# Kernel optimization log

Hardware: AMD Instinct MI355X
Metric: run time of the kernel (lower is better)

The kernel has to match this reference:

```python
import jax, jax.numpy as jnp
import numpy as np

BS, C, H, W = 2, 256, 64, 64
CH = C // 8  # hidden channels = 32


def conv1(x, w, b):
    # 1x1 conv: w [out,in], b [out], x [b,in,H,W] -> [b,out,H,W]
    return jnp.einsum('oc,bchw->bohw', w, x) + b[None, :, None, None]


def setup_inputs() -> dict:
    key = jax.random.key(0)
    ks = jax.random.split(key, 32)
    d = {}
    d['x'] = jax.random.normal(ks[0], (BS, C, H, W), dtype=jnp.float32)
    d['y'] = jax.random.normal(ks[1], (BS, C, H, W), dtype=jnp.float32)
    i = 2
    def wproj(shape):
        nonlocal i
        w = jax.random.normal(ks[i], shape, dtype=jnp.float32) * 0.05
        i += 1
        return w
    for nm in ['f1', 'g1', 'h1', 'f2', 'g2', 'h2']:
        d['w' + nm] = wproj((CH, C))
        d['b' + nm] = jnp.zeros((CH,), dtype=jnp.float32)
    for nm in ['v11', 'v12', 'v21', 'v22']:
        d['w' + nm] = wproj((C, CH))
        d['b' + nm] = jnp.zeros((C,), dtype=jnp.float32)
    for nm in ['o1', 'o2']:
        d['w' + nm] = wproj((C, 2 * C))
        d['b' + nm] = jnp.zeros((C,), dtype=jnp.float32)
    return d


def reference(x, y, wf1, bf1, wg1, bg1, wh1, bh1, wf2, bf2, wg2, bg2, wh2, bh2,
              wv11, bv11, wv12, bv12, wv21, bv21, wv22, bv22, wo1, bo1, wo2, bo2):
    bs, c, h, w = x.shape
    n = h * w
    f1 = conv1(x, wf1, bf1).reshape(bs, -1, n)  # [b,ch,n]
    g1 = conv1(x, wg1, bg1).reshape(bs, -1, n)
    f2 = conv1(y, wf2, bf2).reshape(bs, -1, n)
    g2 = conv1(y, wg2, bg2).reshape(bs, -1, n)
    # attn = softmax(f^T g) over last dim, [b,n,n]
    attn11 = jax.nn.softmax(jnp.einsum('bcn,bcm->bnm', f1, g1), axis=-1)
    attn12 = jax.nn.softmax(jnp.einsum('bcn,bcm->bnm', f1, g2), axis=-1)
    attn21 = jax.nn.softmax(jnp.einsum('bcn,bcm->bnm', f2, g1), axis=-1)
    attn22 = jax.nn.softmax(jnp.einsum('bcn,bcm->bnm', f2, g2), axis=-1)
    h1 = conv1(x, wh1, bh1).reshape(bs, -1, n)  # note: both h from x, as in source
    h2 = conv1(x, wh2, bh2).reshape(bs, -1, n)
    # bmm(h, attn^T): out[c,m] = sum_n h[c,n] attn[m,n]
    v11 = conv1(jnp.einsum('bcn,bmn->bcm', h1, attn11).reshape(bs, -1, h, w), wv11, bv11)
    v12 = conv1(jnp.einsum('bcn,bmn->bcm', h2, attn12).reshape(bs, -1, h, w), wv12, bv12)
    v21 = conv1(jnp.einsum('bcn,bmn->bcm', h1, attn21).reshape(bs, -1, h, w), wv21, bv21)
    v22 = conv1(jnp.einsum('bcn,bmn->bcm', h2, attn22).reshape(bs, -1, h, w), wv22, bv22)
    x_out = x + conv1(jnp.concatenate([v11, v12], axis=1), wo1, bo1)
    y_out = y + conv1(jnp.concatenate([v21, v22], axis=1), wo2, bo2)
    return (x_out, y_out)
```

## Files before the change

### kernel.cpp

```cpp
#include <hip/hip_runtime.h>
#include <hip/hip_bf16.h>
#include <cstdint>

#define N 4096
#define CC 256
#define CH 32
#define L2E 1.4426950408889634f

typedef __attribute__((ext_vector_type(8)))  short short8;
typedef __attribute__((ext_vector_type(16))) float f32x16;
typedef __attribute__((ext_vector_type(4)))  uint32_t u32x4;

#define OFF_WFRAG 0
#define OFF_WEFF  311296
#define OFF_BEFF  344064
#define OFF_QF    344576
#define OFF_KF    606720
#define OFF_VF    868864

__device__ __forceinline__ uint32_t cvtpk_bf16(float lo, float hi) {
  uint32_t r;
  asm("v_cvt_pk_bf16_f32 %0, %1, %2" : "=v"(r) : "v"(lo), "v"(hi));
  return r;
}

__device__ __forceinline__ void rows_to_frags(const float* p, u32x4& lo, u32x4& hi) {
#pragma unroll
  for (int kh = 0; kh < 2; ++kh) {
    int base = kh * 8;
    uint32_t x0 = cvtpk_bf16(p[base + 0], p[base + 1]);
    uint32_t y0 = cvtpk_bf16(p[base + 4], p[base + 5]);
    asm volatile("v_permlane32_swap_b32 %0, %1" : "+v"(x0), "+v"(y0));
    uint32_t x1 = cvtpk_bf16(p[base + 2], p[base + 3]);
    uint32_t y1 = cvtpk_bf16(p[base + 6], p[base + 7]);
    asm volatile("v_permlane32_swap_b32 %0, %1" : "+v"(x1), "+v"(y1));
    u32x4 r; r[0] = x0; r[1] = x1; r[2] = y0; r[3] = y1;
    if (kh == 0) lo = r; else hi = r;
  }
}

__device__ __forceinline__ void attn_step(short8 ak0, short8 ak1, short8 bv0, short8 bv1,
                                          short8 bq0, short8 bq1,
                                          f32x16& ao, float& lacc, const f32x16& zero16) {
  f32x16 sa = __builtin_amdgcn_mfma_f32_32x32x16_bf16(ak0, bq0, zero16, 0, 0, 0);
  sa = __builtin_amdgcn_mfma_f32_32x32x16_bf16(ak1, bq1, sa, 0, 0, 0);
  float p[16];
#pragma unroll
  for (int r = 0; r < 16; ++r) p[r] = __builtin_amdgcn_exp2f(sa[r]);
  float t0 = 0.f, t1 = 0.f;
#pragma unroll
  for (int r = 0; r < 8; ++r) { t0 += p[2 * r]; t1 += p[2 * r + 1]; }
  lacc += t0 + t1;
  u32x4 lo, hi;
  rows_to_frags(p, lo, hi);
  ao = __builtin_amdgcn_mfma_f32_32x32x16_bf16(__builtin_bit_cast(short8, lo), bv0, ao, 0, 0, 0);
  ao = __builtin_amdgcn_mfma_f32_32x32x16_bf16(__builtin_bit_cast(short8, hi), bv1, ao, 0, 0, 0);
}

__global__ void k_prep2(const float* __restrict__ wf1, const float* __restrict__ wg1,
                        const float* __restrict__ wh1, const float* __restrict__ wf2,
                        const float* __restrict__ wg2, const float* __restrict__ wh2,
                        const float* __restrict__ wo1, const float* __restrict__ wo2,
                        const float* __restrict__ wv11, const float* __restrict__ wv12,
                        const float* __restrict__ wv21, const float* __restrict__ wv22,
                        const float* __restrict__ bv11, const float* __restrict__ bv12,
                        const float* __restrict__ bv21, const float* __restrict__ bv22,
                        const float* __restrict__ bo1, const float* __restrict__ bo2,
                        uint16_t* __restrict__ wfragb, float* __restrict__ weff,
                        float* __restrict__ beff) {
  int bid = blockIdx.x;
  if (bid < 192) {
    int idx = bid * 256 + threadIdx.x;
    int q = idx >> 13, kb = (idx >> 9) & 15, l = (idx >> 3) & 63, j = idx & 7;
    int ch = l & 31, c = kb * 16 + (l >> 5) * 8 + j;
    const float* w = q == 0 ? wf1 : q == 1 ? wg1 : q == 2 ? wh1
                   : q == 3 ? wf2 : q == 4 ? wg2 : wh2;
    wfragb[idx] = (uint16_t)cvtpk_bf16(w[ch * CC + c], 0.f);
  } else if (bid < 320) {
    int bid2 = bid - 192;
    int r = bid2 >> 6, ch = bid2 & 63, half = ch >> 5, chp = ch & 31;
    int o = threadIdx.x;
    const float* wv = (r == 0) ? (half ? wv12 : wv11) : (half ? wv22 : wv21);
    const float* wrow = (r == 0 ? wo1 : wo2) + (size_t)o * 512 + half * 256;
    float a[8];
#pragma unroll
    for (int u = 0; u < 8; ++u) a[u] = 0.f;
#pragma unroll 4
    for (int c = 0; c < 256; c += 8) {
#pragma unroll
      for (int u = 0; u < 8; ++u)
        a[u] = fmaf(wrow[c + u], wv[(c + u) * CH + chp], a[u]);
    }
    weff[((size_t)r * 64 + ch) * 256 + o] =
        ((a[0] + a[1]) + (a[2] + a[3])) + ((a[4] + a[5]) + (a[6] + a[7]));
  } else {
    int r = bid - 320;
    int o = threadIdx.x;
    const float* bo  = r == 0 ? bo1 : bo2;
    const float* bva = r == 0 ? bv11 : bv21;
    const float* bvb = r == 0 ? bv12 : bv22;
    const float* wrow = (r == 0 ? wo1 : wo2) + (size_t)o * 512;
    float a[4], b4[4];
#pragma unroll
    for (int u = 0; u < 4; ++u) { a[u] = 0.f; b4[u] = 0.f; }
#pragma unroll 8
    for (int c = 0; c < 256; c += 4) {
#pragma unroll
      for (int u = 0; u < 4; ++u) {
        a[u]  = fmaf(wrow[c + u],       bva[c + u], a[u]);
        b4[u] = fmaf(wrow[c + u + 256], bvb[c + u], b4[u]);
      }
    }
    beff[r * 256 + o] = bo[o] + ((a[0] + a[1]) + (a[2] + a[3]))
                              + ((b4[0] + b4[1]) + (b4[2] + b4[3]));
  }
}

__global__ __launch_bounds__(256) void k_proj(
    const float* __restrict__ x, const float* __restrict__ y,
    const uint16_t* __restrict__ wfragb,
    const float* __restrict__ bf1, const float* __restrict__ bg1, const float* __restrict__ bh1,
    const float* __restrict__ bf2, const float* __restrict__ bg2, const float* __restrict__ bh2,
    uint16_t* __restrict__ Qf, uint16_t* __restrict__ Kf, uint16_t* __restrict__ Vf) {
  int bid = blockIdx.x;
  int w = __builtin_amdgcn_readfirstlane(threadIdx.x >> 6);
  int l = threadIdx.x & 63, l31 = l & 31, l5 = l >> 5;

  int q, ql, b, nt, inst;
  const float* src;
  const float* bias;
  bool isf, isV;
  if (bid < 256) {
    ql = w; b = bid >> 7; nt = bid & 127;
    src = x; inst = 0;
    q = (ql == 3) ? 5 : ql;
    isf = (ql == 0); isV = (ql >= 2);
    bias = ql == 0 ? bf1 : ql == 1 ? bg1 : ql == 2 ? bh1 : bh2;
  } else {
    int u = (bid - 256) * 4 + w;
    int chunk = u >> 1; ql = u & 1;
    b = chunk >> 7; nt = chunk & 127;
    src = y; inst = 1;
    q = 3 + ql;
    isf = (ql == 0); isV = false;
    bias = ql == 0 ? bf2 : bg2;
  }

  const u32x4* wp = (const u32x4*)wfragb + (size_t)q * 16 * 64 + l;
  u32x4 wfr[16];
#pragma unroll
  for (int kb = 0; kb < 16; ++kb) wfr[kb] = wp[kb * 64];

  const float* sp = src + (size_t)b * CC * N + (size_t)(l5 * 8) * N + nt * 32 + l31;
  f32x16 acc;
#pragma unroll
  for (int r = 0; r < 16; ++r) acc[r] = 0.f;

  if (isV) {
#pragma unroll
    for (int kb = 0; kb < 16; ++kb) {
      const float* kp = sp + (size_t)kb * 16 * N;
      float xj[8];
#pragma unroll
      for (int j = 0; j < 8; ++j) xj[j] = kp[(size_t)j * N];
      u32x4 bu;
#pragma unroll
      for (int jh = 0; jh < 4; ++jh) bu[jh] = cvtpk_bf16(xj[2 * jh], xj[2 * jh + 1]);
      acc = __builtin_amdgcn_mfma_f32_32x32x16_bf16(
          __builtin_bit_cast(short8, bu), __builtin_bit_cast(short8, wfr[kb]), acc, 0, 0, 0);
    }
  } else {
#pragma unroll
    for (int kb = 0; kb < 16; ++kb) {
      const float* kp = sp + (size_t)kb * 16 * N;
      float xj[8];
#pragma unroll
      for (int j = 0; j < 8; ++j) xj[j] = kp[(size_t)j * N];
      u32x4 bu;
#pragma unroll
      for (int jh = 0; jh < 4; ++jh) bu[jh] = cvtpk_bf16(xj[2 * jh], xj[2 * jh + 1]);
      acc = __builtin_amdgcn_mfma_f32_32x32x16_bf16(
          __builtin_bit_cast(short8, wfr[kb]), __builtin_bit_cast(short8, bu), acc, 0, 0, 0);
    }
  }

  float p[16];
  if (isV) {
    float bv = bias[l31];
#pragma unroll
    for (int r = 0; r < 16; ++r) p[r] = acc[r] + bv;
  } else {
#pragma unroll
    for (int r = 0; r < 16; ++r) {
      int crow = (r & 3) + 8 * (r >> 2) + 4 * l5;
      float t = acc[r] + bias[crow];
      p[r] = isf ? t * L2E : t;
    }
  }

  u32x4 lo, hi;
  rows_to_frags(p, lo, hi);

  uint16_t* dstb = isV ? Vf : (isf ? Qf : Kf);
  int oinst = isV ? (ql - 2) : inst;
  int b128 = (oinst * 2 + b) * 128 + nt;
  uint32_t* d0 = (uint32_t*)dstb + (size_t)b128 * 512 + l * 4;
  *(u32x4*)d0 = lo;
  *(u32x4*)(d0 + 256) = hi;
}

__global__ __launch_bounds__(512) void k_attnepi(const uint16_t* __restrict__ Qf,
                                                 const uint16_t* __restrict__ Kf,
                                                 const uint16_t* __restrict__ Vf,
                                                 const float* __restrict__ x,
                                                 const float* __restrict__ y,
                                                 const float* __restrict__ weff,
                                                 const float* __restrict__ beff,
                                                 float* __restrict__ out) {
  __shared__ float redAO[2][2][4][32][33];
  __shared__ float redL[2][2][4][32];
  __shared__ float AN[64][65];
  int bid = blockIdx.x;
  int qg = bid & 63, rb = bid >> 6, r = rb >> 1, b = rb & 1;
  int tid = threadIdx.x;
  int w = __builtin_amdgcn_readfirstlane(tid >> 6);
  int ik = w >> 2, kw = w & 3;
  int l = tid & 63, l31 = l & 31, l5 = l >> 5;
  int qt0 = qg * 2, qt1 = qg * 2 + 1;

  const uint16_t* Qp0 = Qf + (size_t)((r * 2 + b) * 128 + qt0) * 1024 + l * 8;
  const uint16_t* Qp1 = Qf + (size_t)((r * 2 + b) * 128 + qt1) * 1024 + l * 8;
  const uint16_t* Kp = Kf + (size_t)((ik * 2 + b) * 128 + kw * 32) * 1024 + l * 8;
  const uint16_t* Vp = Vf + (size_t)((ik * 2 + b) * 128 + kw * 32) * 1024 + l * 8;

  short8 bq00 = *(const short8*)(Qp0);
  short8 bq01 = *(const short8*)(Qp0 + 512);
  short8 bq10 = *(const short8*)(Qp1);
  short8 bq11 = *(const short8*)(Qp1 + 512);

  f32x16 zero16, ao0, ao1;
#pragma unroll
  for (int rr = 0; rr < 16; ++rr) { zero16[rr] = 0.f; ao0[rr] = 0.f; ao1[rr] = 0.f; }
  float lacc0 = 0.f, lacc1 = 0.f;

  for (int t = 0; t < 32; ++t) {
    const uint16_t* kt = Kp + t * 1024;
    short8 ak0 = *(const short8*)(kt);
    short8 ak1 = *(const short8*)(kt + 512);
    const uint16_t* vt = Vp + t * 1024;
    short8 bv0 = *(const short8*)(vt);
    short8 bv1 = *(const short8*)(vt + 512);
    attn_step(ak0, ak1, bv0, bv1, bq00, bq01, ao0, lacc0, zero16);
    attn_step(ak0, ak1, bv0, bv1, bq10, bq11, ao1, lacc1, zero16);
  }

#pragma unroll
  for (int rr = 0; rr < 16; ++rr) {
    int row = (rr & 3) + 8 * (rr >> 2) + 4 * l5;
    redAO[ik][0][kw][row][l31] = ao0[rr];
    redAO[ik][1][kw][row][l31] = ao1[rr];
  }
  lacc0 += __shfl_xor(lacc0, 32);
  lacc1 += __shfl_xor(lacc1, 32);
  if (l < 32) {
    redL[ik][0][kw][l31] = lacc0;
    redL[ik][1][kw][l31] = lacc1;
  }
  __syncthreads();

  {
    int ch = tid >> 3, mblk = tid & 7;
    int qi = mblk >> 2, mq0 = (mblk & 3) * 8;
    int ikc = ch >> 5, chp = ch & 31;
#pragma unroll
    for (int mm = 0; mm < 8; ++mm) {
      int mq = mq0 + mm;
      float L = redL[ikc][qi][0][mq] + redL[ikc][qi][1][mq]
              + redL[ikc][qi][2][mq] + redL[ikc][qi][3][mq];
      float s = redAO[ikc][qi][0][mq][chp] + redAO[ikc][qi][1][mq][chp]
              + redAO[ikc][qi][2][mq][chp] + redAO[ikc][qi][3][mq][chp];
      AN[ch][qi * 32 + mq] = s * __builtin_amdgcn_rcpf(L);
    }
  }
  __syncthreads();

  int m = tid & 63;
  int m0 = qg * 64;
  float acc[32];
#pragma unroll
  for (int j = 0; j < 32; ++j) acc[j] = 0.f;
  const float* wrow = weff + (size_t)(r * 64) * 256 + w * 32;
  for (int ch = 0; ch < 64; ++ch) {
    float a = AN[ch][m];
    const float* wr = wrow + (size_t)ch * 256;
#pragma unroll
    for (int j = 0; j < 32; ++j) acc[j] = fmaf(wr[j], a, acc[j]);
  }
  const float* src = r == 0 ? x : y;
  float* outr = out + (size_t)r * 2 * CC * N;
  const float* be = beff + r * 256 + w * 32;
#pragma unroll
  for (int j = 0; j < 32; ++j) {
    size_t off = ((size_t)b * CC + w * 32 + j) * N + m0 + m;
    outr[off] = src[off] + acc[j] + be[j];
  }
}

extern "C" void kernel_launch(void* const* d_in, const int* in_sizes, int n_in,
                              void* d_out, int out_size, void* d_ws, size_t ws_size,
                              hipStream_t stream) {
  const float* x    = (const float*)d_in[0];
  const float* y    = (const float*)d_in[1];
  const float* wf1  = (const float*)d_in[2];
  const float* bf1  = (const float*)d_in[3];
  const float* wg1  = (const float*)d_in[4];
  const float* bg1  = (const float*)d_in[5];
  const float* wh1  = (const float*)d_in[6];
  const float* bh1  = (const float*)d_in[7];
  const float* wf2  = (const float*)d_in[8];
  const float* bf2  = (const float*)d_in[9];
  const float* wg2  = (const float*)d_in[10];
  const float* bg2  = (const float*)d_in[11];
  const float* wh2  = (const float*)d_in[12];
  const float* bh2  = (const float*)d_in[13];
  const float* wv11 = (const float*)d_in[14];
  const float* bv11 = (const float*)d_in[15];
  const float* wv12 = (const float*)d_in[16];
  const float* bv12 = (const float*)d_in[17];
  const float* wv21 = (const float*)d_in[18];
  const float* bv21 = (const float*)d_in[19];
  const float* wv22 = (const float*)d_in[20];
  const float* bv22 = (const float*)d_in[21];
  const float* wo1  = (const float*)d_in[22];
  const float* bo1  = (const float*)d_in[23];
  const float* wo2  = (const float*)d_in[24];
  const float* bo2  = (const float*)d_in[25];

  float* ws   = (float*)d_ws;
  uint16_t* wfragb = (uint16_t*)(ws + OFF_WFRAG);
  float* weff = ws + OFF_WEFF;
  float* beff = ws + OFF_BEFF;
  uint16_t* Qf = (uint16_t*)(ws + OFF_QF);
  uint16_t* Kf = (uint16_t*)(ws + OFF_KF);
  uint16_t* Vf = (uint16_t*)(ws + OFF_VF);
  float* out  = (float*)d_out;

  k_prep2<<<322, 256, 0, stream>>>(wf1, wg1, wh1, wf2, wg2, wh2, wo1, wo2,
                                   wv11, wv12, wv21, wv22,
                                   bv11, bv12, bv21, bv22, bo1, bo2,
                                   wfragb, weff, beff);
  k_proj<<<384, 256, 0, stream>>>(x, y, wfragb, bf1, bg1, bh1, bf2, bg2, bh2, Qf, Kf, Vf);
  k_attnepi<<<256, 512, 0, stream>>>(Qf, Kf, Vf, x, y, weff, beff, out);
}
```

Measured before the change: 78.90 us.

## Split projection K dimension across wave pairs and store attention reductions as bf16

The projection kernel now splits the 256-channel reduction into two halves handled by separate waves. The halves are combined through shared memory, which doubles the grid and the parallelism per output tile. Separately, the attention epilogue stores its cross-wave partial outputs and normalized values in shared memory as bf16 instead of fp32, shrinking LDS use and possibly raising occupancy. This costs extra precision loss in the reduction and one additional barrier per projection block.

```diff
diff --git a/kernel.cpp b/kernel.cpp
--- a/kernel.cpp
+++ b/kernel.cpp
@@ -22,6 +22,9 @@
   uint32_t r;
   asm("v_cvt_pk_bf16_f32 %0, %1, %2" : "=v"(r) : "v"(lo), "v"(hi));
   return r;
+}
+__device__ __forceinline__ float bf2f(uint16_t u) {
+  return __builtin_bit_cast(float, (uint32_t)u << 16);
 }
 
 __device__ __forceinline__ void rows_to_frags(const float* p, u32x4& lo, u32x4& hi) {
@@ -122,23 +125,27 @@
     const float* __restrict__ bf1, const float* __restrict__ bg1, const float* __restrict__ bh1,
     const float* __restrict__ bf2, const float* __restrict__ bg2, const float* __restrict__ bh2,
     uint16_t* __restrict__ Qf, uint16_t* __restrict__ Kf, uint16_t* __restrict__ Vf) {
+  __shared__ float xch[2][64][17];
   int bid = blockIdx.x;
   int w = __builtin_amdgcn_readfirstlane(threadIdx.x >> 6);
   int l = threadIdx.x & 63, l31 = l & 31, l5 = l >> 5;
 
-  int q, ql, b, nt, inst;
+  int q, ql, b, nt, inst, khalf, pair;
   const float* src;
   const float* bias;
   bool isf, isV;
-  if (bid < 256) {
-    ql = w; b = bid >> 7; nt = bid & 127;
+  if (bid < 512) {
+    int chunk = bid >> 1;
+    ql = (bid & 1) * 2 + (w >> 1); khalf = w & 1; pair = w >> 1;
+    b = chunk >> 7; nt = chunk & 127;
     src = x; inst = 0;
     q = (ql == 3) ? 5 : ql;
     isf = (ql == 0); isV = (ql >= 2);
     bias = ql == 0 ? bf1 : ql == 1 ? bg1 : ql == 2 ? bh1 : bh2;
   } else {
-    int u = (bid - 256) * 4 + w;
-    int chunk = u >> 1; ql = u & 1;
+    int u = (bid - 512) * 4 + w;
+    int task = u >> 1; khalf = u & 1; pair = w >> 1;
+    int chunk = task >> 1; ql = task & 1;
     b = chunk >> 7; nt = chunk & 127;
     src = y; inst = 1;
     q = 3 + ql;
@@ -146,19 +153,19 @@
     bias = ql == 0 ? bf2 : bg2;
   }
 
-  const u32x4* wp = (const u32x4*)wfragb + (size_t)q * 16 * 64 + l;
-  u32x4 wfr[16];
-#pragma unroll
-  for (int kb = 0; kb < 16; ++kb) wfr[kb] = wp[kb * 64];
-
-  const float* sp = src + (size_t)b * CC * N + (size_t)(l5 * 8) * N + nt * 32 + l31;
+  const u32x4* wp = (const u32x4*)wfragb + (size_t)q * 16 * 64 + (size_t)khalf * 8 * 64 + l;
+  u32x4 wfr[8];
+#pragma unroll
+  for (int kb = 0; kb < 8; ++kb) wfr[kb] = wp[kb * 64];
+
+  const float* sp = src + (size_t)b * CC * N + (size_t)(khalf * 128 + l5 * 8) * N + nt * 32 + l31;
   f32x16 acc;
 #pragma unroll
   for (int r = 0; r < 16; ++r) acc[r] = 0.f;
 
   if (isV) {
 #pragma unroll
-    for (int kb = 0; kb < 16; ++kb) {
+    for (int kb = 0; kb < 8; ++kb) {
       const float* kp = sp + (size_t)kb * 16 * N;
       float xj[8];
 #pragma unroll
@@ -171,7 +178,7 @@
     }
   } else {
 #pragma unroll
-    for (int kb = 0; kb < 16; ++kb) {
+    for (int kb = 0; kb < 8; ++kb) {
       const float* kp = sp + (size_t)kb * 16 * N;
       float xj[8];
 #pragma unroll
@@ -183,6 +190,15 @@
           __builtin_bit_cast(short8, wfr[kb]), __builtin_bit_cast(short8, bu), acc, 0, 0, 0);
     }
   }
+
+  if (khalf == 1) {
+#pragma unroll
+    for (int r = 0; r < 16; ++r) xch[pair][l][r] = acc[r];
+  }
+  __syncthreads();
+  if (khalf == 1) return;
+#pragma unroll
+  for (int r = 0; r < 16; ++r) acc[r] += xch[pair][l][r];
 
   float p[16];
   if (isV) {
@@ -217,9 +233,9 @@
                                                  const float* __restrict__ weff,
                                                  const float* __restrict__ beff,
                                                  float* __restrict__ out) {
-  __shared__ float redAO[2][2][4][32][33];
-  __shared__ float redL[2][2][4][32];
-  __shared__ float AN[64][65];
+  __shared__ uint16_t redAO[2][2][4][32][34];
+  __shared__ float    redL[2][2][4][32];
+  __shared__ uint16_t AN[64][66];
   int bid = blockIdx.x;
   int qg = bid & 63, rb = bid >> 6, r = rb >> 1, b = rb & 1;
   int tid = threadIdx.x;
@@ -257,8 +273,8 @@
 #pragma unroll
   for (int rr = 0; rr < 16; ++rr) {
     int row = (rr & 3) + 8 * (rr >> 2) + 4 * l5;
-    redAO[ik][0][kw][row][l31] = ao0[rr];
-    redAO[ik][1][kw][row][l31] = ao1[rr];
+    redAO[ik][0][kw][row][l31] = (uint16_t)cvtpk_bf16(ao0[rr], ao0[rr]);
+    redAO[ik][1][kw][row][l31] = (uint16_t)cvtpk_bf16(ao1[rr], ao1[rr]);
   }
   lacc0 += __shfl_xor(lacc0, 32);
   lacc1 += __shfl_xor(lacc1, 32);
@@ -277,9 +293,10 @@
       int mq = mq0 + mm;
       float L = redL[ikc][qi][0][mq] + redL[ikc][qi][1][mq]
               + redL[ikc][qi][2][mq] + redL[ikc][qi][3][mq];
-      float s = redAO[ikc][qi][0][mq][chp] + redAO[ikc][qi][1][mq][chp]
-              + redAO[ikc][qi][2][mq][chp] + redAO[ikc][qi][3][mq][chp];
-      AN[ch][qi * 32 + mq] = s * __builtin_amdgcn_rcpf(L);
+      float s = bf2f(redAO[ikc][qi][0][mq][chp]) + bf2f(redAO[ikc][qi][1][mq][chp])
+              + bf2f(redAO[ikc][qi][2][mq][chp]) + bf2f(redAO[ikc][qi][3][mq][chp]);
+      float v = s * __builtin_amdgcn_rcpf(L);
+      AN[ch][qi * 32 + mq] = (uint16_t)cvtpk_bf16(v, v);
     }
   }
   __syncthreads();
@@ -291,7 +308,7 @@
   for (int j = 0; j < 32; ++j) acc[j] = 0.f;
   const float* wrow = weff + (size_t)(r * 64) * 256 + w * 32;
   for (int ch = 0; ch < 64; ++ch) {
-    float a = AN[ch][m];
+    float a = bf2f(AN[ch][m]);
     const float* wr = wrow + (size_t)ch * 256;
 #pragma unroll
     for (int j = 0; j < 32; ++j) acc[j] = fmaf(wr[j], a, acc[j]);
@@ -349,6 +366,6 @@
                                    wv11, wv12, wv21, wv22,
                                    bv11, bv12, bv21, bv22, bo1, bo2,
                                    wfragb, weff, beff);
-  k_proj<<<384, 256, 0, stream>>>(x, y, wfragb, bf1, bg1, bh1, bf2, bg2, bh2, Qf, Kf, Vf);
+  k_proj<<<768, 256, 0, stream>>>(x, y, wfragb, bf1, bg1, bh1, bf2, bg2, bh2, Qf, Kf, Vf);
   k_attnepi<<<256, 512, 0, stream>>>(Qf, Kf, Vf, x, y, weff, beff, out);
 }
```

After: 69.12 us. 1.14x faster.
